# Kernel optimization log

Hardware: AMD Instinct MI355X
Metric: run time of the kernel (lower is better)

## Reference

```python
import jax, jax.numpy as jnp
import numpy as np

NONLIN = jnp.tanh  # configurable gate/candidate nonlinearity ('nonlin' init arg)

T, B, I, H = 1024, 64, 256, 512


def setup_inputs() -> dict:
    key = jax.random.key(0)
    k1, k2, k3 = jax.random.split(key, 3)
    s_i = 1.0 / np.sqrt(I)
    s_h = 1.0 / np.sqrt(H)
    return {
        "x": jax.random.normal(k1, (T, B, I), dtype=jnp.float32),
        "Wi": jax.random.normal(k2, (I, 4 * H), dtype=jnp.float32) * s_i,
        "Wh": jax.random.normal(k3, (H, 4 * H), dtype=jnp.float32) * s_h,
        "bi": jnp.zeros((4 * H,), dtype=jnp.float32),
        "bh": jnp.zeros((4 * H,), dtype=jnp.float32),
        "h0": jnp.zeros((B, H), dtype=jnp.float32),
        "c0": jnp.zeros((B, H), dtype=jnp.float32),
    }


def reference(x, Wi, Wh, bi, bh, h0, c0):
    # Precompute input projection for all timesteps in one big GEMM: [T,B,4H]
    x_proj = jnp.einsum('tbi,ig->tbg', x, Wi) + bi

    def step(carry, xp_t):
        h, c = carry
        gates = xp_t + h @ Wh + bh            # [B, 4H]
        i_g, f_g, g_g, o_g = jnp.split(gates, 4, axis=-1)
        i_g = jax.nn.sigmoid(i_g)
        f_g = jax.nn.sigmoid(f_g)
        o_g = jax.nn.sigmoid(o_g)
        g_g = NONLIN(g_g)
        c_new = f_g * c + i_g * g_g
        h_new = o_g * NONLIN(c_new)
        return (h_new, c_new), h_new

    (h_T, c_T), hs = jax.lax.scan(step, (h0, c0), x_proj)
    return hs  # [T, B, H] hidden states for every timestep
```

## Files before the change

kernel.cpp:

```cpp
#include <hip/hip_runtime.h>
#include <math.h>


#define TT      1024
#define BB      64
#define II      256
#define HH      512
#define G4H     2048
#define RPB     16
#define NRG     4
#define NCG     64
#define THREADS 512

typedef short  bf16x8 __attribute__((ext_vector_type(8)));
typedef float  f32x4  __attribute__((ext_vector_type(4)));

__device__ __forceinline__ unsigned int cvtpk_bf16(float a, float b) {
    unsigned int r;
    asm volatile("v_cvt_pk_bf16_f32 %0, %1, %2" : "=v"(r) : "v"(a), "v"(b));
    return r;
}

__device__ __forceinline__ void coh_load4_f4(const float* p0, const float* p1,
                                             const float* p2, const float* p3,
                                             float4& a, float4& b,
                                             float4& c, float4& d) {
    asm volatile(
        "global_load_dwordx4 %0, %4, off sc0 sc1\n\t"
        "global_load_dwordx4 %1, %5, off sc0 sc1\n\t"
        "global_load_dwordx4 %2, %6, off sc0 sc1\n\t"
        "global_load_dwordx4 %3, %7, off sc0 sc1\n\t"
        "s_waitcnt vmcnt(0)"
        : "=&v"(a), "=&v"(b), "=&v"(c), "=&v"(d)
        : "v"(p0), "v"(p1), "v"(p2), "v"(p3)
        : "memory");
}
__device__ __forceinline__ void coh_store_f(float* p, float v) {
    asm volatile("global_store_dword %0, %1, off sc0 sc1"
                 :: "v"(p), "v"(v) : "memory");
}
__device__ __forceinline__ void coh_store_u(unsigned int* p, unsigned int v) {
    asm volatile("global_store_dword %0, %1, off sc0 sc1"
                 :: "v"(p), "v"(v) : "memory");
}
__device__ __forceinline__ float fast_tanh(float v) {
    const float e = __expf(-2.0f * fabsf(v));
    const float r = (1.0f - e) / (1.0f + e);
    return v < 0.0f ? -r : r;
}
__device__ __forceinline__ float sigm(float v) {
    return 1.0f / (1.0f + __expf(-v));
}

__device__ __forceinline__ void cvt_frag(float4 v0, float4 v1,
                                         uint4& hi, uint4& lo) {
    hi.x = cvtpk_bf16(v0.x, v0.y);
    hi.y = cvtpk_bf16(v0.z, v0.w);
    hi.z = cvtpk_bf16(v1.x, v1.y);
    hi.w = cvtpk_bf16(v1.z, v1.w);
    lo.x = cvtpk_bf16(v0.x - __uint_as_float(hi.x << 16),
                      v0.y - __uint_as_float(hi.x & 0xffff0000u));
    lo.y = cvtpk_bf16(v0.z - __uint_as_float(hi.y << 16),
                      v0.w - __uint_as_float(hi.y & 0xffff0000u));
    lo.z = cvtpk_bf16(v1.x - __uint_as_float(hi.z << 16),
                      v1.y - __uint_as_float(hi.z & 0xffff0000u));
    lo.w = cvtpk_bf16(v1.z - __uint_as_float(hi.w << 16),
                      v1.w - __uint_as_float(hi.w & 0xffff0000u));
}

__global__ void init_flags(unsigned int* f) { f[threadIdx.x] = 0; }

__global__ __launch_bounds__(THREADS) void lstm_persist(
    const float* __restrict__ x,
    const float* __restrict__ Wi,
    const float* __restrict__ Wh,
    const float* __restrict__ bi,
    const float* __restrict__ bh,
    const float* __restrict__ h0p,
    const float* __restrict__ c0p,
    float* __restrict__ out,
    unsigned int* __restrict__ flags)
{
    const int tid   = threadIdx.x;
    const int cg    = blockIdx.x & 63;
    const int rg    = blockIdx.x >> 6;
    const int row0  = rg * RPB;
    const int cell0 = cg * 8;
    const int wv    = tid >> 6;
    const int lane  = tid & 63;
    const int n2    = wv >> 2;
    const int k4    = wv & 3;

    __shared__ uint4 aFH[24 * 64];
    __shared__ uint4 aFL[24 * 64];
    __shared__ float red[8 * 64 * 4];
    __shared__ float c_lds[RPB][8];

    const int s_ls = tid & 63;
    const int s_r  = s_ls & 15;
    const int s_kb = (tid >> 6) * 32 + ((s_ls >> 4) & 3) * 8;

    bf16x8 wH[6], wL[6];
    {
        const int col = n2 * 16 + (lane & 15);
        const int J   = (col >> 3) * HH + cell0 + (col & 7);
        #pragma unroll
        for (int s = 0; s < 6; ++s) {
            const int kk = (s < 2) ? (k4 * 2 + s) : (8 + k4 * 4 + (s - 2));
            const int kb = kk * 32 + (lane >> 4) * 8;
            float w[8];
            #pragma unroll
            for (int e = 0; e < 8; ++e) {
                const int k = kb + e;
                w[e] = (k < II) ? Wi[(size_t)k * G4H + J]
                                : Wh[(size_t)(k - II) * G4H + J];
            }
            uint4 hi, lo;
            cvt_frag(make_float4(w[0], w[1], w[2], w[3]),
                     make_float4(w[4], w[5], w[6], w[7]), hi, lo);
            wH[s] = *(bf16x8*)&hi;
            wL[s] = *(bf16x8*)&lo;
        }
    }

    float b4[4];
    if (tid < 128) {
        const int r = tid >> 3, m8 = tid & 7;
        #pragma unroll
        for (int g = 0; g < 4; ++g)
            b4[g] = bi[g * HH + cell0 + m8] + bh[g * HH + cell0 + m8];
        c_lds[r][m8] = c0p[(size_t)(row0 + r) * HH + cell0 + m8];
    }

    {
        const float* xr = x + (size_t)(row0 + s_r) * II + s_kb;
        uint4 hi, lo;
        cvt_frag(*(const float4*)xr, *(const float4*)(xr + 4), hi, lo);
        aFH[tid] = hi; aFL[tid] = lo;

        const float* hr = h0p + (size_t)(row0 + s_r) * HH + s_kb;
        cvt_frag(*(const float4*)hr, *(const float4*)(hr + 4), hi, lo);
        aFH[512 + tid] = hi; aFL[512 + tid] = lo;
        cvt_frag(*(const float4*)(hr + 256), *(const float4*)(hr + 260), hi, lo);
        aFH[1024 + tid] = hi; aFL[1024 + tid] = lo;
    }
    __syncthreads();

    f32x4 acc = {0.f, 0.f, 0.f, 0.f};
    #pragma unroll
    for (int q = 0; q < 2; ++q) {
        const int kk = k4 * 2 + q;
        const bf16x8 ah = *(const bf16x8*)&aFH[kk * 64 + lane];
        const bf16x8 al = *(const bf16x8*)&aFL[kk * 64 + lane];
        acc = __builtin_amdgcn_mfma_f32_16x16x32_bf16(ah, wH[q], acc, 0, 0, 0);
        acc = __builtin_amdgcn_mfma_f32_16x16x32_bf16(ah, wL[q], acc, 0, 0, 0);
        acc = __builtin_amdgcn_mfma_f32_16x16x32_bf16(al, wH[q], acc, 0, 0, 0);
    }

    unsigned int* myflag   = flags + (rg * NCG + cg) * 4;
    unsigned int* pollbase = flags + (rg * NCG + lane) * 4;

    for (int t = 0; t < TT; ++t) {
        const bool more = (t + 1 < TT);

        float4 xv0, xv1;
        if (more) {
            const float* xr = x + ((size_t)(t + 1) * BB + row0 + s_r) * II + s_kb;
            xv0 = *(const float4*)xr;
            xv1 = *(const float4*)(xr + 4);
        }

        #pragma unroll
        for (int q = 0; q < 4; ++q) {
            const int kk = 8 + k4 * 4 + q;
            const bf16x8 ah = *(const bf16x8*)&aFH[kk * 64 + lane];
            const bf16x8 al = *(const bf16x8*)&aFL[kk * 64 + lane];
            acc = __builtin_amdgcn_mfma_f32_16x16x32_bf16(ah, wH[2 + q], acc, 0, 0, 0);
            acc = __builtin_amdgcn_mfma_f32_16x16x32_bf16(ah, wL[2 + q], acc, 0, 0, 0);
            acc = __builtin_amdgcn_mfma_f32_16x16x32_bf16(al, wH[2 + q], acc, 0, 0, 0);
        }

        ((f32x4*)red)[wv * 64 + lane] = acc;
        if (more) {
            uint4 hi, lo;
            cvt_frag(xv0, xv1, hi, lo);
            aFH[tid] = hi; aFL[tid] = lo;
        }
        __syncthreads();

        if (tid < 128) {
            const int r = tid >> 3, m8 = tid & 7;
            const int lane_c_base = 16 * (r >> 2);
            const int reg = r & 3;
            float g4[4];
            #pragma unroll
            for (int g = 0; g < 4; ++g) {
                const int col = g * 8 + m8;
                const int nn  = col >> 4, cl = col & 15;
                const int lc  = cl + lane_c_base;
                float s = b4[g];
                #pragma unroll
                for (int p = 0; p < 4; ++p)
                    s += red[((nn * 4 + p) * 64 + lc) * 4 + reg];
                g4[g] = s;
            }
            const float ig = sigm(g4[0]);
            const float fg = sigm(g4[1]);
            const float gg = fast_tanh(g4[2]);
            const float og = sigm(g4[3]);
            const float cn = fg * c_lds[r][m8] + ig * gg;
            c_lds[r][m8] = cn;
            coh_store_f(out + ((size_t)t * BB + row0 + r) * HH + cell0 + m8,
                        og * fast_tanh(cn));
        }

        asm volatile("s_waitcnt vmcnt(0) lgkmcnt(0)" ::: "memory");
        __syncthreads();
        if (more) {
            if (tid == 0) coh_store_u(myflag, (unsigned int)(t + 1));

            acc = (f32x4){0.f, 0.f, 0.f, 0.f};
            #pragma unroll
            for (int q = 0; q < 2; ++q) {
                const int kk = k4 * 2 + q;
                const bf16x8 ah = *(const bf16x8*)&aFH[kk * 64 + lane];
                const bf16x8 al = *(const bf16x8*)&aFL[kk * 64 + lane];
                acc = __builtin_amdgcn_mfma_f32_16x16x32_bf16(ah, wH[q], acc, 0, 0, 0);
                acc = __builtin_amdgcn_mfma_f32_16x16x32_bf16(ah, wL[q], acc, 0, 0, 0);
                acc = __builtin_amdgcn_mfma_f32_16x16x32_bf16(al, wH[q], acc, 0, 0, 0);
            }

            if (wv == 0) {
                const unsigned int tgt = (unsigned int)(t + 1);
                for (;;) {
                    const unsigned int v =
                        __hip_atomic_load(pollbase, __ATOMIC_RELAXED,
                                          __HIP_MEMORY_SCOPE_AGENT);
                    if (__all(v >= tgt)) break;
                    __builtin_amdgcn_s_sleep(1);
                }
            }
            __syncthreads();

            {
                const float* hr = out + (size_t)t * BB * HH
                                  + (size_t)(row0 + s_r) * HH + s_kb;
                float4 v0, v1, v2, v3;
                coh_load4_f4(hr, hr + 4, hr + 256, hr + 260, v0, v1, v2, v3);
                uint4 hi, lo;
                cvt_frag(v0, v1, hi, lo);
                aFH[512 + tid] = hi; aFL[512 + tid] = lo;
                cvt_frag(v2, v3, hi, lo);
                aFH[1024 + tid] = hi; aFL[1024 + tid] = lo;
            }
            __syncthreads();
        }
    }
}

extern "C" void kernel_launch(void* const* d_in, const int* in_sizes, int n_in,
                              void* d_out, int out_size, void* d_ws, size_t ws_size,
                              hipStream_t stream) {
    const float* x  = (const float*)d_in[0];
    const float* Wi = (const float*)d_in[1];
    const float* Wh = (const float*)d_in[2];
    const float* bi = (const float*)d_in[3];
    const float* bh = (const float*)d_in[4];
    const float* h0 = (const float*)d_in[5];
    const float* c0 = (const float*)d_in[6];
    float* out = (float*)d_out;
    unsigned int* flags = (unsigned int*)d_ws;

    init_flags<<<1, 1024, 0, stream>>>(flags);

    void* args[] = { (void*)&x, (void*)&Wi, (void*)&Wh, (void*)&bi,
                     (void*)&bh, (void*)&h0, (void*)&c0, (void*)&out,
                     (void*)&flags };
    hipError_t e = hipLaunchCooperativeKernel((const void*)lstm_persist,
                                              dim3(NRG * NCG), dim3(THREADS),
                                              args, 0, stream);
    if (e != hipSuccess) {
        (void)hipGetLastError();
        lstm_persist<<<dim3(NRG * NCG), dim3(THREADS), 0, stream>>>(
            x, Wi, Wh, bi, bh, h0, c0, out, flags);
    }
}
```

Baseline: 4.390 ms.

## Replace per-block flag barrier with value+step tagged hidden-state exchange buffer

Each hidden value is now written into a double-buffered workspace as a (value, step) pair with one coherent 8-byte store. Consumers poll their own slice directly until every tag matches the current step, so the flag stores, the block-wide waitcnt+syncthreads before signalling, and the separate wave-0 poll plus its barrier are all removed. This cuts cross-block synchronisation latency on the serial timestep critical path. In exchange every thread polls with eight 16-byte loads, which doubles the traffic of the exchange. Correctness relies on the 8-byte store being observed atomically.

```diff
diff --git a/kernel.cpp b/kernel.cpp
--- a/kernel.cpp
+++ b/kernel.cpp
@@ -20,27 +20,8 @@
     asm volatile("v_cvt_pk_bf16_f32 %0, %1, %2" : "=v"(r) : "v"(a), "v"(b));
     return r;
 }
-
-__device__ __forceinline__ void coh_load4_f4(const float* p0, const float* p1,
-                                             const float* p2, const float* p3,
-                                             float4& a, float4& b,
-                                             float4& c, float4& d) {
-    asm volatile(
-        "global_load_dwordx4 %0, %4, off sc0 sc1\n\t"
-        "global_load_dwordx4 %1, %5, off sc0 sc1\n\t"
-        "global_load_dwordx4 %2, %6, off sc0 sc1\n\t"
-        "global_load_dwordx4 %3, %7, off sc0 sc1\n\t"
-        "s_waitcnt vmcnt(0)"
-        : "=&v"(a), "=&v"(b), "=&v"(c), "=&v"(d)
-        : "v"(p0), "v"(p1), "v"(p2), "v"(p3)
-        : "memory");
-}
-__device__ __forceinline__ void coh_store_f(float* p, float v) {
-    asm volatile("global_store_dword %0, %1, off sc0 sc1"
-                 :: "v"(p), "v"(v) : "memory");
-}
-__device__ __forceinline__ void coh_store_u(unsigned int* p, unsigned int v) {
-    asm volatile("global_store_dword %0, %1, off sc0 sc1"
+__device__ __forceinline__ void coh_store_u2(uint2* p, uint2 v) {
+    asm volatile("global_store_dwordx2 %0, %1, off sc0 sc1"
                  :: "v"(p), "v"(v) : "memory");
 }
 __device__ __forceinline__ float fast_tanh(float v) {
@@ -68,7 +49,9 @@
                       v1.w - __uint_as_float(hi.w & 0xffff0000u));
 }
 
-__global__ void init_flags(unsigned int* f) { f[threadIdx.x] = 0; }
+__global__ void init_hx(uint4* p) {
+    p[blockIdx.x * 256 + threadIdx.x] = (uint4){0u, 0u, 0u, 0u};
+}
 
 __global__ __launch_bounds__(THREADS) void lstm_persist(
     const float* __restrict__ x,
@@ -79,7 +62,7 @@
     const float* __restrict__ h0p,
     const float* __restrict__ c0p,
     float* __restrict__ out,
-    unsigned int* __restrict__ flags)
+    uint2* __restrict__ hx)
 {
     const int tid   = threadIdx.x;
     const int cg    = blockIdx.x & 63;
@@ -156,9 +139,6 @@
         acc = __builtin_amdgcn_mfma_f32_16x16x32_bf16(ah, wL[q], acc, 0, 0, 0);
         acc = __builtin_amdgcn_mfma_f32_16x16x32_bf16(al, wH[q], acc, 0, 0, 0);
     }
-
-    unsigned int* myflag   = flags + (rg * NCG + cg) * 4;
-    unsigned int* pollbase = flags + (rg * NCG + lane) * 4;
 
     for (int t = 0; t < TT; ++t) {
         const bool more = (t + 1 < TT);
@@ -210,15 +190,17 @@
             const float og = sigm(g4[3]);
             const float cn = fg * c_lds[r][m8] + ig * gg;
             c_lds[r][m8] = cn;
-            coh_store_f(out + ((size_t)t * BB + row0 + r) * HH + cell0 + m8,
-                        og * fast_tanh(cn));
-        }
-
-        asm volatile("s_waitcnt vmcnt(0) lgkmcnt(0)" ::: "memory");
-        __syncthreads();
+            const float hv = og * fast_tanh(cn);
+            out[((size_t)t * BB + row0 + r) * HH + cell0 + m8] = hv;
+            if (more) {
+                uint2 pr; pr.x = __float_as_uint(hv);
+                pr.y = (unsigned int)(t + 1);
+                coh_store_u2(&hx[((size_t)(t & 1) * BB + row0 + r) * HH
+                                 + cell0 + m8], pr);
+            }
+        }
+
         if (more) {
-            if (tid == 0) coh_store_u(myflag, (unsigned int)(t + 1));
-
             acc = (f32x4){0.f, 0.f, 0.f, 0.f};
             #pragma unroll
             for (int q = 0; q < 2; ++q) {
@@ -230,27 +212,54 @@
                 acc = __builtin_amdgcn_mfma_f32_16x16x32_bf16(al, wH[q], acc, 0, 0, 0);
             }
 
-            if (wv == 0) {
-                const unsigned int tgt = (unsigned int)(t + 1);
-                for (;;) {
-                    const unsigned int v =
-                        __hip_atomic_load(pollbase, __ATOMIC_RELAXED,
-                                          __HIP_MEMORY_SCOPE_AGENT);
-                    if (__all(v >= tgt)) break;
-                    __builtin_amdgcn_s_sleep(1);
-                }
-            }
-            __syncthreads();
+            const uint2* hb = hx + ((size_t)(t & 1) * BB + row0 + s_r) * HH + s_kb;
+            uint4 q0, q1, q2, q3, q4, q5, q6, q7;
+            const unsigned int tgt = (unsigned int)(t + 1);
+            for (;;) {
+                asm volatile(
+                    "global_load_dwordx4 %0, %8, off sc0 sc1\n\t"
+                    "global_load_dwordx4 %1, %8, off offset:16 sc0 sc1\n\t"
+                    "global_load_dwordx4 %2, %8, off offset:32 sc0 sc1\n\t"
+                    "global_load_dwordx4 %3, %8, off offset:48 sc0 sc1\n\t"
+                    "global_load_dwordx4 %4, %8, off offset:2048 sc0 sc1\n\t"
+                    "global_load_dwordx4 %5, %8, off offset:2064 sc0 sc1\n\t"
+                    "global_load_dwordx4 %6, %8, off offset:2080 sc0 sc1\n\t"
+                    "global_load_dwordx4 %7, %8, off offset:2096 sc0 sc1\n\t"
+                    "s_waitcnt vmcnt(0)"
+                    : "=&v"(q0), "=&v"(q1), "=&v"(q2), "=&v"(q3),
+                      "=&v"(q4), "=&v"(q5), "=&v"(q6), "=&v"(q7)
+                    : "v"(hb)
+                    : "memory");
+                const bool ok =
+                    (q0.y == tgt) & (q0.w == tgt) & (q1.y == tgt) & (q1.w == tgt) &
+                    (q2.y == tgt) & (q2.w == tgt) & (q3.y == tgt) & (q3.w == tgt) &
+                    (q4.y == tgt) & (q4.w == tgt) & (q5.y == tgt) & (q5.w == tgt) &
+                    (q6.y == tgt) & (q6.w == tgt) & (q7.y == tgt) & (q7.w == tgt);
+                if (ok) break;
+                __builtin_amdgcn_s_sleep(1);
+            }
 
             {
-                const float* hr = out + (size_t)t * BB * HH
-                                  + (size_t)(row0 + s_r) * HH + s_kb;
-                float4 v0, v1, v2, v3;
-                coh_load4_f4(hr, hr + 4, hr + 256, hr + 260, v0, v1, v2, v3);
                 uint4 hi, lo;
-                cvt_frag(v0, v1, hi, lo);
+                const float4 a0 = make_float4(__uint_as_float(q0.x),
+                                              __uint_as_float(q0.z),
+                                              __uint_as_float(q1.x),
+                                              __uint_as_float(q1.z));
+                const float4 a1 = make_float4(__uint_as_float(q2.x),
+                                              __uint_as_float(q2.z),
+                                              __uint_as_float(q3.x),
+                                              __uint_as_float(q3.z));
+                cvt_frag(a0, a1, hi, lo);
                 aFH[512 + tid] = hi; aFL[512 + tid] = lo;
-                cvt_frag(v2, v3, hi, lo);
+                const float4 b0 = make_float4(__uint_as_float(q4.x),
+                                              __uint_as_float(q4.z),
+                                              __uint_as_float(q5.x),
+                                              __uint_as_float(q5.z));
+                const float4 b1 = make_float4(__uint_as_float(q6.x),
+                                              __uint_as_float(q6.z),
+                                              __uint_as_float(q7.x),
+                                              __uint_as_float(q7.z));
+                cvt_frag(b0, b1, hi, lo);
                 aFH[1024 + tid] = hi; aFL[1024 + tid] = lo;
             }
             __syncthreads();
@@ -269,19 +278,19 @@
     const float* h0 = (const float*)d_in[5];
     const float* c0 = (const float*)d_in[6];
     float* out = (float*)d_out;
-    unsigned int* flags = (unsigned int*)d_ws;
-
-    init_flags<<<1, 1024, 0, stream>>>(flags);
+    uint2* hx = (uint2*)d_ws;
+
+    init_hx<<<128, 256, 0, stream>>>((uint4*)d_ws);
 
     void* args[] = { (void*)&x, (void*)&Wi, (void*)&Wh, (void*)&bi,
                      (void*)&bh, (void*)&h0, (void*)&c0, (void*)&out,
-                     (void*)&flags };
+                     (void*)&hx };
     hipError_t e = hipLaunchCooperativeKernel((const void*)lstm_persist,
                                               dim3(NRG * NCG), dim3(THREADS),
                                               args, 0, stream);
     if (e != hipSuccess) {
         (void)hipGetLastError();
         lstm_persist<<<dim3(NRG * NCG), dim3(THREADS), 0, stream>>>(
-            x, Wi, Wh, bi, bh, h0, c0, out, flags);
-    }
-}
+            x, Wi, Wh, bi, bh, h0, c0, out, hx);
+    }
+}
```

Result: slower. 9.239 ms (+110.5%).
